# Kernel tuning notes

Hardware: AMD Instinct MI355X
Metric: run time of the kernel (lower is better)

The kernel has to match this reference:

```python
import jax, jax.numpy as jnp
import numpy as np

KD, KH, KW = 3, 3, 3
C = 64

def setup_inputs() -> dict:
    key = jax.random.key(0)
    kx, kw = jax.random.split(key)
    x = jax.random.normal(kx, (4, 16, 112, 112, C), dtype=jnp.float32)
    # One 3x3x3 filter per channel; DHWIO layout with I=in_per_group=1, O=C
    w = jax.random.normal(kw, (KD, KH, KW, 1, C), dtype=jnp.float32) * 0.1
    return {"x": x, "w": w}

def reference(x, w) -> jnp.ndarray:
    # Depthwise 3D conv: feature_group_count=C makes each output channel the
    # conv of the matching input channel with its own [3,3,3] kernel, which is
    # exactly the per-channel Conv3D(filters=1) loop + concat in the original.
    return jax.lax.conv_general_dilated(
        x, w,
        window_strides=(1, 1, 1),
        padding="SAME",
        dimension_numbers=("NDHWC", "DHWIO", "NDHWC"),
        feature_group_count=C,
    )
```

## Files before the change

### kernel.cpp

```cpp
#include <hip/hip_runtime.h>

#define N_ 4
#define D_ 16
#define H_ 112
#define W_ 112
#define C_ 64

#define DO_ 2
#define HO_ 2
#define DT_ (D_ / DO_)
#define HTILES (H_ / HO_)
#define WAVES_PER_BLOCK 4
#define HGROUPS (HTILES / WAVES_PER_BLOCK)
#define WSPLIT 4
#define WQ (W_ / WSPLIT)
#define NWG (N_ * DT_ * HGROUPS * WSPLIT)
#define CB (C_ * 4)

__device__ float zpage[W_ * C_];

template <int U, int DR, int HR, int KWM>
__device__ __forceinline__ void stream_fma(float (&acc)[3][2][2],
                                           const float (&wt)[3][3][3],
                                           float v) {
  constexpr int iN = U % 3;
  constexpr int iM = (U + 5) % 3;
  constexpr int iO = (U + 4) % 3;
#pragma unroll
  for (int od = (DR >= 2 ? DR - 2 : 0); od <= (DR < 1 ? DR : 1); ++od)
#pragma unroll
    for (int oh = (HR >= 2 ? HR - 2 : 0); oh <= (HR < 1 ? HR : 1); ++oh) {
      if (KWM & 1) acc[iN][od][oh] += v * wt[DR - od][HR - oh][0];
      if (KWM & 2) acc[iM][od][oh] += v * wt[DR - od][HR - oh][1];
      if (KWM & 4) acc[iO][od][oh] += v * wt[DR - od][HR - oh][2];
    }
}

#define FL(U, M, DR, HR)                                        \
  stream_fma<U, DR, HR, M>(acc, wt, pf[DR][HR]);                \
  pf[DR][HR] = *(const float*)(bx[DR][HR] + vb);
#define F_(U, M, DR, HR) stream_fma<U, DR, HR, M>(acc, wt, pf[DR][HR]);
#define L_(DR, HR) pf[DR][HR] = *(const float*)(bx[DR][HR] + vb);

#define FMA_LOAD_ALL(U, M)                                      \
  FL(U,M,0,0) FL(U,M,0,1) FL(U,M,0,2) FL(U,M,0,3)               \
  FL(U,M,1,0) FL(U,M,1,1) FL(U,M,1,2) FL(U,M,1,3)               \
  FL(U,M,2,0) FL(U,M,2,1) FL(U,M,2,2) FL(U,M,2,3)               \
  FL(U,M,3,0) FL(U,M,3,1) FL(U,M,3,2) FL(U,M,3,3)

#define FMA_ALL(U, M)                                           \
  F_(U,M,0,0) F_(U,M,0,1) F_(U,M,0,2) F_(U,M,0,3)               \
  F_(U,M,1,0) F_(U,M,1,1) F_(U,M,1,2) F_(U,M,1,3)               \
  F_(U,M,2,0) F_(U,M,2,1) F_(U,M,2,2) F_(U,M,2,3)               \
  F_(U,M,3,0) F_(U,M,3,1) F_(U,M,3,2) F_(U,M,3,3)

#define LOAD_ALL()                                              \
  L_(0,0) L_(0,1) L_(0,2) L_(0,3) L_(1,0) L_(1,1) L_(1,2) L_(1,3) \
  L_(2,0) L_(2,1) L_(2,2) L_(2,3) L_(3,0) L_(3,1) L_(3,2) L_(3,3)

#define STORE4(U)                                                             \
  *(float*)(ox[0][0] + (vb - 2*CB)) = acc[(U+4)%3][0][0]; acc[(U+4)%3][0][0] = 0.f; \
  *(float*)(ox[0][1] + (vb - 2*CB)) = acc[(U+4)%3][0][1]; acc[(U+4)%3][0][1] = 0.f; \
  *(float*)(ox[1][0] + (vb - 2*CB)) = acc[(U+4)%3][1][0]; acc[(U+4)%3][1][0] = 0.f; \
  *(float*)(ox[1][1] + (vb - 2*CB)) = acc[(U+4)%3][1][1]; acc[(U+4)%3][1][1] = 0.f;

__global__ __launch_bounds__(256, 4)
void dwconv3d_kernel(const float* __restrict__ x,
                     const float* __restrict__ wgt,
                     float* __restrict__ out) {
    int b = blockIdx.x;
    b = (b & 7) * (NWG / 8) + (b >> 3);
    const int wh = b % WSPLIT; b /= WSPLIT;
    const int hg = b % HGROUPS; b /= HGROUPS;
    const int dt = b % DT_;     b /= DT_;
    const int n  = b;

    const int c   = threadIdx.x & 63;
    const int wid = __builtin_amdgcn_readfirstlane(threadIdx.x >> 6);

    const int d0 = dt * DO_;
    const int h0 = (hg * WAVES_PER_BLOCK + wid) * HO_;
    const int w0 = wh * WQ;

    float wt[3][3][3];
#pragma unroll
    for (int kd = 0; kd < 3; ++kd)
#pragma unroll
      for (int kh = 0; kh < 3; ++kh)
#pragma unroll
        for (int kw = 0; kw < 3; ++kw)
          wt[kd][kh][kw] = wgt[((kd * 3 + kh) * 3 + kw) * C_ + c];

    const char* bx[4][4];
#pragma unroll
    for (int dr = 0; dr < 4; ++dr) {
      const int d = d0 - 1 + dr;
#pragma unroll
      for (int hr = 0; hr < 4; ++hr) {
        const int h = h0 - 1 + hr;
        if (d >= 0 && d < D_ && h >= 0 && h < H_)
          bx[dr][hr] = (const char*)(x + (size_t)((n * D_ + d) * H_ + h) * W_ * C_);
        else
          bx[dr][hr] = (const char*)zpage;
      }
    }

    char* ox[2][2];
#pragma unroll
    for (int od = 0; od < 2; ++od)
#pragma unroll
      for (int oh = 0; oh < 2; ++oh)
        ox[od][oh] = (char*)(out +
            (size_t)((n * D_ + d0 + od) * H_ + (h0 + oh)) * W_ * C_);

    float pf[4][4];
    float acc[3][2][2];
#pragma unroll
    for (int i = 0; i < 3; ++i)
#pragma unroll
      for (int od = 0; od < 2; ++od)
#pragma unroll
        for (int oh = 0; oh < 2; ++oh) acc[i][od][oh] = 0.f;

    unsigned vb = (unsigned)(w0 * CB) + (unsigned)(c * 4);
    const bool wend = (w0 + WQ < W_);

    if (w0) {
#pragma unroll
      for (int dr = 0; dr < 4; ++dr)
#pragma unroll
        for (int hr = 0; hr < 4; ++hr)
          pf[dr][hr] = *(const float*)(bx[dr][hr] + (vb - CB));
      FMA_LOAD_ALL(0, 1)
    } else {
      LOAD_ALL()
    }
    vb += CB;
    FMA_LOAD_ALL(1, 3) vb += CB;
    FMA_LOAD_ALL(2, 7) STORE4(2) vb += CB;
    FMA_LOAD_ALL(3, 7) STORE4(3) vb += CB;
    FMA_LOAD_ALL(4, 7) STORE4(4) vb += CB;
    FMA_LOAD_ALL(5, 7) STORE4(5) vb += CB;
#pragma unroll 1
    for (int it = 0; it < 3; ++it) {
      FMA_LOAD_ALL(0, 7) STORE4(0) vb += CB;
      FMA_LOAD_ALL(1, 7) STORE4(1) vb += CB;
      FMA_LOAD_ALL(2, 7) STORE4(2) vb += CB;
      FMA_LOAD_ALL(3, 7) STORE4(3) vb += CB;
      FMA_LOAD_ALL(4, 7) STORE4(4) vb += CB;
      FMA_LOAD_ALL(5, 7) STORE4(5) vb += CB;
    }
    FMA_LOAD_ALL(0, 7) STORE4(0) vb += CB;
    FMA_LOAD_ALL(1, 7) STORE4(1) vb += CB;
    FMA_LOAD_ALL(2, 7) STORE4(2) vb += CB;
    FMA_LOAD_ALL(3, 7) STORE4(3) vb += CB;
    if (wend) {
      FMA_LOAD_ALL(4, 6)
    } else {
      FMA_ALL(4, 6)
    }
    STORE4(4) vb += CB;
    if (wend) { FMA_ALL(5, 4) }
    STORE4(5)
}

extern "C" void kernel_launch(void* const* d_in, const int* in_sizes, int n_in,
                              void* d_out, int out_size, void* d_ws, size_t ws_size,
                              hipStream_t stream) {
    const float* x   = (const float*)d_in[0];
    const float* wgt = (const float*)d_in[1];
    float* out = (float*)d_out;

    dim3 grid(NWG);
    dim3 block(256);
    dwconv3d_kernel<<<grid, block, 0, stream>>>(x, wgt, out);
}
```

Before: 370.8 us.

## Stage shared input rows in LDS to deduplicate halo loads across waves

Instead of each wave streaming its own 4x4 grid of input rows directly from global memory, the block cooperatively loads the 4 depth x 10 height rows it needs into LDS in float4 chunks of four W positions. Waves then read their 16 values per W step from LDS. This removes the redundant global loads caused by overlapping H halos between the four waves. In exchange it adds barriers and s_waitcnt per stage, loses the register-prefetch overlap of global loads with FMAs, and uses about 40 KB of LDS per block, which may limit occupancy.

```diff
diff --git a/kernel.cpp b/kernel.cpp
--- a/kernel.cpp
+++ b/kernel.cpp
@@ -16,6 +16,7 @@
 #define WQ (W_ / WSPLIT)
 #define NWG (N_ * DT_ * HGROUPS * WSPLIT)
 #define CB (C_ * 4)
+#define ROWB (W_ * CB)
 
 __device__ float zpage[W_ * C_];
 
@@ -36,27 +37,12 @@
     }
 }
 
-#define FL(U, M, DR, HR)                                        \
-  stream_fma<U, DR, HR, M>(acc, wt, pf[DR][HR]);                \
-  pf[DR][HR] = *(const float*)(bx[DR][HR] + vb);
-#define F_(U, M, DR, HR) stream_fma<U, DR, HR, M>(acc, wt, pf[DR][HR]);
-#define L_(DR, HR) pf[DR][HR] = *(const float*)(bx[DR][HR] + vb);
-
-#define FMA_LOAD_ALL(U, M)                                      \
-  FL(U,M,0,0) FL(U,M,0,1) FL(U,M,0,2) FL(U,M,0,3)               \
-  FL(U,M,1,0) FL(U,M,1,1) FL(U,M,1,2) FL(U,M,1,3)               \
-  FL(U,M,2,0) FL(U,M,2,1) FL(U,M,2,2) FL(U,M,2,3)               \
-  FL(U,M,3,0) FL(U,M,3,1) FL(U,M,3,2) FL(U,M,3,3)
-
-#define FMA_ALL(U, M)                                           \
+#define F_(U, M, DR, HR) stream_fma<U, DR, HR, M>(acc, wt, lv[DR][HR]);
+#define F16(U, M)                                               \
   F_(U,M,0,0) F_(U,M,0,1) F_(U,M,0,2) F_(U,M,0,3)               \
   F_(U,M,1,0) F_(U,M,1,1) F_(U,M,1,2) F_(U,M,1,3)               \
   F_(U,M,2,0) F_(U,M,2,1) F_(U,M,2,2) F_(U,M,2,3)               \
   F_(U,M,3,0) F_(U,M,3,1) F_(U,M,3,2) F_(U,M,3,3)
-
-#define LOAD_ALL()                                              \
-  L_(0,0) L_(0,1) L_(0,2) L_(0,3) L_(1,0) L_(1,1) L_(1,2) L_(1,3) \
-  L_(2,0) L_(2,1) L_(2,2) L_(2,3) L_(3,0) L_(3,1) L_(3,2) L_(3,3)
 
 #define STORE4(U)                                                             \
   *(float*)(ox[0][0] + (vb - 2*CB)) = acc[(U+4)%3][0][0]; acc[(U+4)%3][0][0] = 0.f; \
@@ -64,10 +50,48 @@
   *(float*)(ox[1][0] + (vb - 2*CB)) = acc[(U+4)%3][1][0]; acc[(U+4)%3][1][0] = 0.f; \
   *(float*)(ox[1][1] + (vb - 2*CB)) = acc[(U+4)%3][1][1]; acc[(U+4)%3][1][1] = 0.f;
 
+#define DSTEP(U, M, Q, DOST)                                          \
+  {                                                                   \
+    float lv[4][4];                                                   \
+    _Pragma("unroll") for (int dr = 0; dr < 4; ++dr)                  \
+      _Pragma("unroll") for (int hr = 0; hr < 4; ++hr)                \
+        lv[dr][hr] = lp[(((dr)*10 + (hr))*4 + (Q)) * 64];             \
+    F16(U, M)                                                         \
+    if (DOST) { STORE4(U) }                                           \
+    vb += CB;                                                         \
+  }
+
+#define STAGE_SS(T)                                                   \
+  {                                                                   \
+    int off = vb16 + ((w0 - 1 + 4*(T)) * CB);                         \
+    off = off < 0 ? 0 : off;                                          \
+    off = off > (ROWB - 16) ? (ROWB - 16) : off;                      \
+    _Pragma("unroll") for (int j = 0; j < 10; ++j) {                  \
+      float4 v = *(const float4*)(sb[j] + off);                       \
+      *(float4*)(sw + j*1024) = v;                                    \
+    }                                                                 \
+  }
+
+#define SYNC_IN()                                                            \
+  asm volatile("s_waitcnt vmcnt(0) lgkmcnt(0)" ::: "memory");                \
+  __builtin_amdgcn_s_barrier();                                              \
+  asm volatile("" ::: "memory");
+#define SYNC_OUT()                                                           \
+  asm volatile("" ::: "memory");                                             \
+  __builtin_amdgcn_s_barrier();
+
+#define SS4(T, U0,M0,S0, U1,M1,S1, U2,M2,S2, U3,M3,S3)  \
+  STAGE_SS(T) SYNC_IN()                                  \
+  DSTEP(U0,M0,0,S0) DSTEP(U1,M1,1,S1)                    \
+  DSTEP(U2,M2,2,S2) DSTEP(U3,M3,3,S3)                    \
+  SYNC_OUT()
+
 __global__ __launch_bounds__(256, 4)
 void dwconv3d_kernel(const float* __restrict__ x,
                      const float* __restrict__ wgt,
                      float* __restrict__ out) {
+    __shared__ float lds[40][4][64];
+
     int b = blockIdx.x;
     b = (b & 7) * (NWG / 8) + (b >> 3);
     const int wh = b % WSPLIT; b /= WSPLIT;
@@ -81,6 +105,7 @@
     const int d0 = dt * DO_;
     const int h0 = (hg * WAVES_PER_BLOCK + wid) * HO_;
     const int w0 = wh * WQ;
+    const bool wend = (w0 + WQ < W_);
 
     float wt[3][3][3];
 #pragma unroll
@@ -91,19 +116,22 @@
         for (int kw = 0; kw < 3; ++kw)
           wt[kd][kh][kw] = wgt[((kd * 3 + kh) * 3 + kw) * C_ + c];
 
-    const char* bx[4][4];
+    const char* sb[10];
+    {
+      const int d = d0 - 1 + wid;
+      const bool dv = (d >= 0) && (d < D_);
 #pragma unroll
-    for (int dr = 0; dr < 4; ++dr) {
-      const int d = d0 - 1 + dr;
-#pragma unroll
-      for (int hr = 0; hr < 4; ++hr) {
-        const int h = h0 - 1 + hr;
-        if (d >= 0 && d < D_ && h >= 0 && h < H_)
-          bx[dr][hr] = (const char*)(x + (size_t)((n * D_ + d) * H_ + h) * W_ * C_);
-        else
-          bx[dr][hr] = (const char*)zpage;
+      for (int j = 0; j < 10; ++j) {
+        const int h = hg * 8 - 1 + j;
+        const bool hv = (h >= 0) && (h < H_);
+        sb[j] = (dv && hv)
+            ? (const char*)(x + (size_t)((n * D_ + d) * H_ + h) * W_ * C_)
+            : (const char*)zpage;
       }
     }
+
+    char* sw = (char*)lds + wid * 10240 + c * 16;
+    const float* lp = (const float*)((const char*)lds + wid * 2048 + c * 4);
 
     char* ox[2][2];
 #pragma unroll
@@ -113,7 +141,6 @@
         ox[od][oh] = (char*)(out +
             (size_t)((n * D_ + d0 + od) * H_ + (h0 + oh)) * W_ * C_);
 
-    float pf[4][4];
     float acc[3][2][2];
 #pragma unroll
     for (int i = 0; i < 3; ++i)
@@ -122,46 +149,22 @@
 #pragma unroll
         for (int oh = 0; oh < 2; ++oh) acc[i][od][oh] = 0.f;
 
+    const int vb16 = c * 16;
     unsigned vb = (unsigned)(w0 * CB) + (unsigned)(c * 4);
-    const bool wend = (w0 + WQ < W_);
 
-    if (w0) {
-#pragma unroll
-      for (int dr = 0; dr < 4; ++dr)
-#pragma unroll
-        for (int hr = 0; hr < 4; ++hr)
-          pf[dr][hr] = *(const float*)(bx[dr][hr] + (vb - CB));
-      FMA_LOAD_ALL(0, 1)
-    } else {
-      LOAD_ALL()
+    if (w0) { SS4(0, 0,1,0, 1,3,0, 2,7,1, 3,7,1) }
+    else    { SS4(0, 0,0,0, 1,3,0, 2,7,1, 3,7,1) }
+#pragma unroll 1
+    for (int r = 0; r < 2; ++r) {
+      const int t = 1 + r * 3;
+      SS4(t,     4,7,1, 5,7,1, 0,7,1, 1,7,1)
+      SS4(t + 1, 2,7,1, 3,7,1, 4,7,1, 5,7,1)
+      SS4(t + 2, 0,7,1, 1,7,1, 2,7,1, 3,7,1)
     }
-    vb += CB;
-    FMA_LOAD_ALL(1, 3) vb += CB;
-    FMA_LOAD_ALL(2, 7) STORE4(2) vb += CB;
-    FMA_LOAD_ALL(3, 7) STORE4(3) vb += CB;
-    FMA_LOAD_ALL(4, 7) STORE4(4) vb += CB;
-    FMA_LOAD_ALL(5, 7) STORE4(5) vb += CB;
-#pragma unroll 1
-    for (int it = 0; it < 3; ++it) {
-      FMA_LOAD_ALL(0, 7) STORE4(0) vb += CB;
-      FMA_LOAD_ALL(1, 7) STORE4(1) vb += CB;
-      FMA_LOAD_ALL(2, 7) STORE4(2) vb += CB;
-      FMA_LOAD_ALL(3, 7) STORE4(3) vb += CB;
-      FMA_LOAD_ALL(4, 7) STORE4(4) vb += CB;
-      FMA_LOAD_ALL(5, 7) STORE4(5) vb += CB;
-    }
-    FMA_LOAD_ALL(0, 7) STORE4(0) vb += CB;
-    FMA_LOAD_ALL(1, 7) STORE4(1) vb += CB;
-    FMA_LOAD_ALL(2, 7) STORE4(2) vb += CB;
-    FMA_LOAD_ALL(3, 7) STORE4(3) vb += CB;
-    if (wend) {
-      FMA_LOAD_ALL(4, 6)
-    } else {
-      FMA_ALL(4, 6)
-    }
-    STORE4(4) vb += CB;
-    if (wend) { FMA_ALL(5, 4) }
-    STORE4(5)
+    STAGE_SS(7) SYNC_IN()
+    DSTEP(4, 6, 0, 1)
+    if (wend) { DSTEP(5, 4, 1, 1) }
+    else      { DSTEP(5, 0, 1, 1) }
 }
 
 extern "C" void kernel_launch(void* const* d_in, const int* in_sizes, int n_in,
```

Result: slower. 429.4 us (+15.8%).
